# Kernel tuning notes

Hardware: AMD Instinct MI355X
Metric: run time of the kernel (lower is better)

Reference implementation:

```python
import jax, jax.numpy as jnp
import numpy as np
from jax import lax

A_PLUS = 0.01
A_MINUS = 0.01
TAU_PLUS = 20.0
TAU_MINUS = 20.0
W_MAX = 1.0
W_MIN = 0.0

B, T, PRE_N, POST_N = 16, 128, 2048, 2048


def setup_inputs() -> dict:
    key = jax.random.key(0)
    k1, k2, k3 = jax.random.split(key, 3)
    weights = jax.random.uniform(k1, (POST_N, PRE_N), dtype=jnp.float32)
    pre_spikes = jax.random.uniform(k2, (B, T, PRE_N), dtype=jnp.float32)
    post_spikes = jax.random.uniform(k3, (B, T, POST_N), dtype=jnp.float32)
    return {"weights": weights, "pre_spikes": pre_spikes,
            "post_spikes": post_spikes, "dt": 1}


def compute_trace(spikes, tau, dt):
    # Faithful to torch loop: trace[:,0,:] = 0; trace[t] = decay*trace[t-1] + spikes[t] for t>=1
    decay = jnp.exp(jnp.float32(-dt / tau))
    s_tb = jnp.swapaxes(spikes, 0, 1)  # [T, B, N]
    init = jnp.zeros_like(s_tb[0])

    def step(carry, s_t):
        tr = decay * carry + s_t
        return tr, tr

    _, tr = lax.scan(step, init, s_tb[1:])          # [T-1, B, N]
    tr = jnp.concatenate([init[None], tr], axis=0)  # [T, B, N]
    return jnp.swapaxes(tr, 0, 1)                   # [B, T, N]


def reference(weights, pre_spikes, post_spikes, dt):
    batch = pre_spikes.shape[0]
    pre_trace = compute_trace(pre_spikes, TAU_PLUS, dt)
    post_trace = compute_trace(post_spikes, TAU_MINUS, dt)

    # sum over t of mean over batch of outer products -> single contraction over (b, t)
    # ltp[q,p] = A_plus * sum_t mean_b post_spikes[b,t,q] * pre_trace[b,t,p]
    ltp = A_PLUS * jnp.einsum('btq,btp->qp', post_spikes, pre_trace) / batch
    # ltd[q,p] = -A_minus * sum_t mean_b post_trace[b,t,q] * pre_spikes[b,t,p]
    ltd = -A_MINUS * jnp.einsum('btq,btp->qp', post_trace, pre_spikes) / batch

    # softbound weight dependence (constant in t, distributes over the sum)
    w_factor = (W_MAX - weights) * (weights - W_MIN) / ((W_MAX - W_MIN) / 2) ** 2
    delta_w = w_factor * (ltp + ltd)
    return delta_w
```

## Files before the change

kernel.cpp:

```cpp
#include <hip/hip_runtime.h>
#include <hip/hip_bf16.h>


typedef __attribute__((ext_vector_type(8))) short bf16x8;
typedef __attribute__((ext_vector_type(16))) float f32x16;

#define GN 2048
#define KTOT 2048
#define A_SCALE (0.01f / 16.0f)
#define FST 68
#define ZST 66

#define GLOAD_LDS16(gp, lp) \
    __builtin_amdgcn_global_load_lds((const __attribute__((address_space(1))) void*)(gp), \
                                     (__attribute__((address_space(3))) void*)(lp), 16, 0, 0)

__device__ __forceinline__ unsigned bf16bits(float x) {
    __hip_bfloat16 h = __float2bfloat16(x);
    return (unsigned)*(unsigned short*)&h;
}

__global__ __launch_bounds__(256, 4) void trace_kernel(
    const float* __restrict__ pre,
    const float* __restrict__ post,
    const int* __restrict__ dtp,
    __hip_bfloat16* __restrict__ AT,
    __hip_bfloat16* __restrict__ BT)
{
    __shared__ float fbuf[128 * FST];
    __hip_bfloat16* zbuf = (__hip_bfloat16*)fbuf;

    const int tid = threadIdx.x;
    const int w   = tid >> 6;
    const int l   = tid & 63;
    const int nq  = tid & 15;
    const int tl  = tid >> 4;
    const int n0  = blockIdx.x * 64;
    const int b   = blockIdx.y;
    const int a   = blockIdx.z;

    int di = dtp[0];
    float dtf = (di > 0 && di < 1000000) ? (float)di : *(const float*)dtp;
    const float decay = __expf(-dtf / 20.0f);

    if (a == 0) {
        #pragma unroll
        for (int pass = 0; pass < 8; ++pass) {
            const int t = pass * 16 + tl;
            float4 v = *(const float4*)&post[((size_t)b * 128 + t) * GN + n0 + 4 * nq];
            uint2 pk;
            pk.x = bf16bits(v.x) | (bf16bits(v.y) << 16);
            pk.y = bf16bits(v.z) | (bf16bits(v.w) << 16);
            *(uint2*)&zbuf[t * ZST + 4 * nq] = pk;
        }
        __syncthreads();
    } else {
        #pragma unroll
        for (int pass = 0; pass < 8; ++pass) {
            const int t = pass * 16 + tl;
            float4 v = *(const float4*)&pre[((size_t)b * 128 + t) * GN + n0 + 4 * nq];
            *(float4*)&fbuf[t * FST + 4 * nq] = v;
        }
        __syncthreads();

        const int t0 = 32 * w;
        float carry = 0.0f;
        #pragma unroll 8
        for (int t = 1; t < t0; ++t)
            carry = decay * carry + fbuf[t * FST + l];
        float z[32];
        #pragma unroll
        for (int j = 0; j < 32; ++j) {
            const int t = t0 + j;
            if (t >= 1) carry = decay * carry + fbuf[t * FST + l];
            z[j] = carry;
        }
        float bc = 0.0f;
        #pragma unroll 8
        for (int t = 127; t >= t0 + 32; --t)
            bc = decay * bc + fbuf[t * FST + l];
        #pragma unroll
        for (int j = 31; j >= 0; --j) {
            const int t = t0 + j;
            bc = decay * bc + fbuf[t * FST + l];
            if (t >= 1) z[j] -= bc;
        }
        __syncthreads();
        #pragma unroll
        for (int j = 0; j < 32; ++j)
            zbuf[(t0 + j) * ZST + l] = __float2bfloat16(z[j]);
        __syncthreads();
    }

    __hip_bfloat16* dst = (a == 0) ? AT : BT;
    #pragma unroll
    for (int j = 0; j < 4; ++j) {
        const int c  = tid + 256 * j;
        const int n  = c >> 4;
        const int tc = c & 15;
        unsigned int vv[8];
        #pragma unroll
        for (int i = 0; i < 8; ++i)
            vv[i] = *(const unsigned short*)&zbuf[(8 * tc + i) * ZST + n];
        uint4 pk;
        pk.x = vv[0] | (vv[1] << 16);
        pk.y = vv[2] | (vv[3] << 16);
        pk.z = vv[4] | (vv[5] << 16);
        pk.w = vv[6] | (vv[7] << 16);
        *(uint4*)(dst + (size_t)(n0 + n) * KTOT + b * 128 + tc * 8) = pk;
    }
}

__global__ __launch_bounds__(512, 4) void stdp_gemm(
    const __hip_bfloat16* __restrict__ AT,
    const __hip_bfloat16* __restrict__ BT,
    const float* __restrict__ W,
    float* __restrict__ out)
{
    __shared__ alignas(16) char smem[73728];

    const int tid  = threadIdx.x;
    const int lane = tid & 63;
    const int wv8  = tid >> 6;
    const int wr   = wv8 >> 1;
    const int wc   = wv8 & 1;
    const int RM   = blockIdx.y * 128;
    const int CN   = blockIdx.x * 64;
    const int l31  = lane & 31;
    const int hi   = lane >> 5;

    const int cS   = wv8 * 64 + lane;
    const int rS   = cS >> 3;
    const int sS   = cS & 7;
    const int kc0  = sS ^ (rS & 7);
    const int kc1  = sS ^ ((rS + 64) & 7);
    const __hip_bfloat16* srcA0 = AT + (size_t)(RM + rS)      * KTOT + kc0 * 8;
    const __hip_bfloat16* srcA1 = AT + (size_t)(RM + rS + 64) * KTOT + kc1 * 8;
    const __hip_bfloat16* srcB  = BT + (size_t)(CN + rS)      * KTOT + kc0 * 8;
    const int dS = wv8 * 1024;

#define STAGE(BUF, kstep) do {                                   \
        char* bb_ = (BUF);                                       \
        const int ke_ = (kstep) * 64;                            \
        GLOAD_LDS16(srcA0 + ke_, bb_ + dS);                      \
        GLOAD_LDS16(srcA1 + ke_, bb_ + 8192 + dS);               \
        GLOAD_LDS16(srcB  + ke_, bb_ + 16384 + dS);              \
    } while (0)

    const int ra = wr * 32 + l31;
    const int rb = wc * 32 + l31;

    f32x16 acc = {};

#define COMPUTE(BUF) do {                                                       \
        const __hip_bfloat16* Ab_ = (const __hip_bfloat16*)(BUF);               \
        const __hip_bfloat16* Bb_ = (const __hip_bfloat16*)((BUF) + 16384);     \
        bf16x8 av_[4], bv_[4];                                                  \
        _Pragma("unroll")                                                       \
        for (int ks_ = 0; ks_ < 4; ++ks_) {                                     \
            const int ja_ = (ks_ * 2 + hi) ^ (ra & 7);                          \
            const int jb_ = (ks_ * 2 + hi) ^ (rb & 7);                          \
            av_[ks_] = *(const bf16x8*)(Ab_ + ra * 64 + ja_ * 8);               \
            bv_[ks_] = *(const bf16x8*)(Bb_ + rb * 64 + jb_ * 8);               \
        }                                                                       \
        _Pragma("unroll")                                                       \
        for (int ks_ = 0; ks_ < 4; ++ks_)                                       \
            acc = __builtin_amdgcn_mfma_f32_32x32x16_bf16(av_[ks_], bv_[ks_],   \
                                                          acc, 0, 0, 0);        \
    } while (0)

#define WAITBAR(N) do {                                          \
        asm volatile("s_waitcnt vmcnt(" #N ")" ::: "memory");    \
        __builtin_amdgcn_s_barrier();                            \
        __builtin_amdgcn_sched_barrier(0);                       \
    } while (0)

    char* B0 = smem;
    char* B1 = smem + 24576;
    char* B2 = smem + 49152;

    STAGE(B0, 0);
    STAGE(B1, 1);
    WAITBAR(3);

    for (int hb = 0; hb < 30; hb += 3) {
        STAGE(B2, hb + 2); COMPUTE(B0); WAITBAR(3);
        STAGE(B0, hb + 3); COMPUTE(B1); WAITBAR(3);
        STAGE(B1, hb + 4); COMPUTE(B2); WAITBAR(3);
    }
    COMPUTE(B0);
    WAITBAR(0);
    COMPUTE(B1);

#undef STAGE
#undef COMPUTE
#undef WAITBAR

    const int p = CN + wc * 32 + l31;
    #pragma unroll
    for (int r = 0; r < 16; ++r) {
        const int q = RM + wr * 32 + (r & 3) + 8 * (r >> 2) + 4 * hi;
        const float w  = W[(size_t)q * GN + p];
        const float wf = 4.0f * w * (1.0f - w);
        out[(size_t)q * GN + p] = wf * A_SCALE * acc[r];
    }
}

extern "C" void kernel_launch(void* const* d_in, const int* in_sizes, int n_in,
                              void* d_out, int out_size, void* d_ws, size_t ws_size,
                              hipStream_t stream) {
    const float* W    = (const float*)d_in[0];
    const float* pre  = (const float*)d_in[1];
    const float* post = (const float*)d_in[2];
    const int*   dt   = (const int*)d_in[3];
    float* out = (float*)d_out;

    __hip_bfloat16* AT = (__hip_bfloat16*)d_ws;
    __hip_bfloat16* BT = AT + (size_t)GN * KTOT;

    trace_kernel<<<dim3(32, 16, 2), 256, 0, stream>>>(pre, post, dt, AT, BT);
    stdp_gemm<<<dim3(32, 16), 512, 0, stream>>>(AT, BT, W, out);
}
```

Before: 119.3 us.

## Enlarge GEMM block tile to 128x128 with 2x2 MFMA tiles per wave

The GEMM block tile grows from 128x64 to 128x128, and each of 4 waves now computes a 64x64 sub-tile with four 32x32 accumulators instead of 8 waves each doing one 32x32 tile. This is meant to raise operand reuse per LDS load and halve global traffic for A per output. In exchange LDS use rises to 96KB per block and register pressure grows, which lowers occupancy. The grid shrinks to 256 blocks, which may underfill the 256 CUs.

```diff
diff --git a/kernel.cpp b/kernel.cpp
--- a/kernel.cpp
+++ b/kernel.cpp
@@ -111,62 +111,75 @@
     }
 }
 
-__global__ __launch_bounds__(512, 4) void stdp_gemm(
+__global__ __launch_bounds__(256) void stdp_gemm(
     const __hip_bfloat16* __restrict__ AT,
     const __hip_bfloat16* __restrict__ BT,
     const float* __restrict__ W,
     float* __restrict__ out)
 {
-    __shared__ alignas(16) char smem[73728];
+    __shared__ alignas(16) char smem[98304];
 
     const int tid  = threadIdx.x;
     const int lane = tid & 63;
-    const int wv8  = tid >> 6;
-    const int wr   = wv8 >> 1;
-    const int wc   = wv8 & 1;
+    const int wv   = tid >> 6;
+    const int wr   = wv >> 1;
+    const int wc   = wv & 1;
     const int RM   = blockIdx.y * 128;
-    const int CN   = blockIdx.x * 64;
+    const int CN   = blockIdx.x * 128;
     const int l31  = lane & 31;
     const int hi   = lane >> 5;
 
-    const int cS   = wv8 * 64 + lane;
-    const int rS   = cS >> 3;
-    const int sS   = cS & 7;
-    const int kc0  = sS ^ (rS & 7);
-    const int kc1  = sS ^ ((rS + 64) & 7);
-    const __hip_bfloat16* srcA0 = AT + (size_t)(RM + rS)      * KTOT + kc0 * 8;
-    const __hip_bfloat16* srcA1 = AT + (size_t)(RM + rS + 64) * KTOT + kc1 * 8;
-    const __hip_bfloat16* srcB  = BT + (size_t)(CN + rS)      * KTOT + kc0 * 8;
-    const int dS = wv8 * 1024;
+    const int rS = (wv << 3) + (lane >> 3);
+    const int kc = (lane & 7) ^ ((lane >> 3) & 7);
+    const __hip_bfloat16* sA0 = AT + (size_t)(RM + rS)      * KTOT + kc * 8;
+    const __hip_bfloat16* sA1 = AT + (size_t)(RM + rS + 32) * KTOT + kc * 8;
+    const __hip_bfloat16* sA2 = AT + (size_t)(RM + rS + 64) * KTOT + kc * 8;
+    const __hip_bfloat16* sA3 = AT + (size_t)(RM + rS + 96) * KTOT + kc * 8;
+    const __hip_bfloat16* sB0 = BT + (size_t)(CN + rS)      * KTOT + kc * 8;
+    const __hip_bfloat16* sB1 = BT + (size_t)(CN + rS + 32) * KTOT + kc * 8;
+    const __hip_bfloat16* sB2 = BT + (size_t)(CN + rS + 64) * KTOT + kc * 8;
+    const __hip_bfloat16* sB3 = BT + (size_t)(CN + rS + 96) * KTOT + kc * 8;
+    const int dS = wv * 1024;
 
 #define STAGE(BUF, kstep) do {                                   \
         char* bb_ = (BUF);                                       \
         const int ke_ = (kstep) * 64;                            \
-        GLOAD_LDS16(srcA0 + ke_, bb_ + dS);                      \
-        GLOAD_LDS16(srcA1 + ke_, bb_ + 8192 + dS);               \
-        GLOAD_LDS16(srcB  + ke_, bb_ + 16384 + dS);              \
+        GLOAD_LDS16(sA0 + ke_, bb_ + dS);                        \
+        GLOAD_LDS16(sA1 + ke_, bb_ + 4096 + dS);                 \
+        GLOAD_LDS16(sA2 + ke_, bb_ + 8192 + dS);                 \
+        GLOAD_LDS16(sA3 + ke_, bb_ + 12288 + dS);                \
+        GLOAD_LDS16(sB0 + ke_, bb_ + 16384 + dS);                \
+        GLOAD_LDS16(sB1 + ke_, bb_ + 20480 + dS);                \
+        GLOAD_LDS16(sB2 + ke_, bb_ + 24576 + dS);                \
+        GLOAD_LDS16(sB3 + ke_, bb_ + 28672 + dS);                \
     } while (0)
 
-    const int ra = wr * 32 + l31;
-    const int rb = wc * 32 + l31;
-
-    f32x16 acc = {};
+    const int ra0 = wr * 64 + l31;
+    const int ra1 = ra0 + 32;
+    const int rb0 = wc * 64 + l31;
+    const int rb1 = rb0 + 32;
+
+    f32x16 acc00 = {}, acc01 = {}, acc10 = {}, acc11 = {};
 
 #define COMPUTE(BUF) do {                                                       \
         const __hip_bfloat16* Ab_ = (const __hip_bfloat16*)(BUF);               \
         const __hip_bfloat16* Bb_ = (const __hip_bfloat16*)((BUF) + 16384);     \
-        bf16x8 av_[4], bv_[4];                                                  \
+        bf16x8 a0_[4], a1_[4], b0_[4], b1_[4];                                  \
         _Pragma("unroll")                                                       \
         for (int ks_ = 0; ks_ < 4; ++ks_) {                                     \
-            const int ja_ = (ks_ * 2 + hi) ^ (ra & 7);                          \
-            const int jb_ = (ks_ * 2 + hi) ^ (rb & 7);                          \
-            av_[ks_] = *(const bf16x8*)(Ab_ + ra * 64 + ja_ * 8);               \
-            bv_[ks_] = *(const bf16x8*)(Bb_ + rb * 64 + jb_ * 8);               \
+            const int j_ = ks_ * 2 + hi;                                        \
+            a0_[ks_] = *(const bf16x8*)(Ab_ + ra0 * 64 + ((j_ ^ (ra0 & 7)) * 8)); \
+            a1_[ks_] = *(const bf16x8*)(Ab_ + ra1 * 64 + ((j_ ^ (ra1 & 7)) * 8)); \
+            b0_[ks_] = *(const bf16x8*)(Bb_ + rb0 * 64 + ((j_ ^ (rb0 & 7)) * 8)); \
+            b1_[ks_] = *(const bf16x8*)(Bb_ + rb1 * 64 + ((j_ ^ (rb1 & 7)) * 8)); \
         }                                                                       \
         _Pragma("unroll")                                                       \
-        for (int ks_ = 0; ks_ < 4; ++ks_)                                       \
-            acc = __builtin_amdgcn_mfma_f32_32x32x16_bf16(av_[ks_], bv_[ks_],   \
-                                                          acc, 0, 0, 0);        \
+        for (int ks_ = 0; ks_ < 4; ++ks_) {                                     \
+            acc00 = __builtin_amdgcn_mfma_f32_32x32x16_bf16(a0_[ks_], b0_[ks_], acc00, 0, 0, 0); \
+            acc01 = __builtin_amdgcn_mfma_f32_32x32x16_bf16(a0_[ks_], b1_[ks_], acc01, 0, 0, 0); \
+            acc10 = __builtin_amdgcn_mfma_f32_32x32x16_bf16(a1_[ks_], b0_[ks_], acc10, 0, 0, 0); \
+            acc11 = __builtin_amdgcn_mfma_f32_32x32x16_bf16(a1_[ks_], b1_[ks_], acc11, 0, 0, 0); \
+        }                                                                       \
     } while (0)
 
 #define WAITBAR(N) do {                                          \
@@ -176,17 +189,17 @@
     } while (0)
 
     char* B0 = smem;
-    char* B1 = smem + 24576;
-    char* B2 = smem + 49152;
+    char* B1 = smem + 32768;
+    char* B2 = smem + 65536;
 
     STAGE(B0, 0);
     STAGE(B1, 1);
-    WAITBAR(3);
+    WAITBAR(8);
 
     for (int hb = 0; hb < 30; hb += 3) {
-        STAGE(B2, hb + 2); COMPUTE(B0); WAITBAR(3);
-        STAGE(B0, hb + 3); COMPUTE(B1); WAITBAR(3);
-        STAGE(B1, hb + 4); COMPUTE(B2); WAITBAR(3);
+        STAGE(B2, hb + 2); COMPUTE(B0); WAITBAR(8);
+        STAGE(B0, hb + 3); COMPUTE(B1); WAITBAR(8);
+        STAGE(B1, hb + 4); COMPUTE(B2); WAITBAR(8);
     }
     COMPUTE(B0);
     WAITBAR(0);
@@ -196,13 +209,21 @@
 #undef COMPUTE
 #undef WAITBAR
 
-    const int p = CN + wc * 32 + l31;
     #pragma unroll
-    for (int r = 0; r < 16; ++r) {
-        const int q = RM + wr * 32 + (r & 3) + 8 * (r >> 2) + 4 * hi;
-        const float w  = W[(size_t)q * GN + p];
-        const float wf = 4.0f * w * (1.0f - w);
-        out[(size_t)q * GN + p] = wf * A_SCALE * acc[r];
+    for (int i = 0; i < 2; ++i) {
+        #pragma unroll
+        for (int j = 0; j < 2; ++j) {
+            const f32x16 a = (i == 0) ? (j == 0 ? acc00 : acc01)
+                                      : (j == 0 ? acc10 : acc11);
+            const int p = CN + wc * 64 + j * 32 + l31;
+            #pragma unroll
+            for (int r = 0; r < 16; ++r) {
+                const int q = RM + wr * 64 + i * 32 + (r & 3) + 8 * (r >> 2) + 4 * hi;
+                const float w  = W[(size_t)q * GN + p];
+                const float wf = 4.0f * w * (1.0f - w);
+                out[(size_t)q * GN + p] = wf * A_SCALE * a[r];
+            }
+        }
     }
 }
 
@@ -219,5 +240,5 @@
     __hip_bfloat16* BT = AT + (size_t)GN * KTOT;
 
     trace_kernel<<<dim3(32, 16, 2), 256, 0, stream>>>(pre, post, dt, AT, BT);
-    stdp_gemm<<<dim3(32, 16), 512, 0, stream>>>(AT, BT, W, out);
-}
+    stdp_gemm<<<dim3(16, 16), 256, 0, stream>>>(AT, BT, W, out);
+}
```

Measured after the change: 120.2 us. Within noise of the previous version (+0.8%).
